# Optimization experiments

Hardware: AMD Instinct MI355X
Metric: run time of the kernel (lower is better)

The kernel has to match this reference:

```python
import jax, jax.numpy as jnp
import numpy as np

D_EMBED = 1024


def setup_inputs() -> dict:
    key = jax.random.key(0)
    ks = jax.random.split(key, 8)
    B, S, D = 8, 2048, D_EMBED
    scale = 1.0 / np.sqrt(D)
    return {
        "embeddings": jax.random.normal(ks[0], (B, S, D), dtype=jnp.float32),
        "mask": jnp.zeros((B, S, S), dtype=jnp.float32),
        "Wq": jax.random.normal(ks[1], (D, D), dtype=jnp.float32) * scale,
        "bq": jax.random.normal(ks[2], (D,), dtype=jnp.float32) * 0.02,
        "Wk": jax.random.normal(ks[3], (D, D), dtype=jnp.float32) * scale,
        "bk": jax.random.normal(ks[4], (D,), dtype=jnp.float32) * 0.02,
        "Wv": jax.random.normal(ks[5], (D, D), dtype=jnp.float32) * scale,
        "bv": jax.random.normal(ks[6], (D,), dtype=jnp.float32) * 0.02,
    }


def reference(embeddings, mask, Wq, bq, Wk, bk, Wv, bv):
    # torch Linear: y = x @ W.T + b
    q = jnp.einsum('bsd,ed->bse', embeddings, Wq) + bq
    k = jnp.einsum('bsd,ed->bse', embeddings, Wk) + bk
    v = jnp.einsum('bsd,ed->bse', embeddings, Wv) + bv
    scores = jnp.einsum('bqd,bkd->bqk', q, k)
    # NOTE: faithful to source — mask added BEFORE scaling by 1/sqrt(d)
    scores = (scores + mask) * (1.0 / jnp.sqrt(jnp.float32(q.shape[-1])))
    attn = jax.nn.softmax(scores, axis=-1)
    return jnp.einsum('bqk,bkd->bqd', attn, v)
```

## Files before the change

### kernel.cpp

```cpp
#include <hip/hip_runtime.h>


#define B_SZ 8
#define SEQ  2048
#define DIM  1024
#define MROWS (B_SZ * SEQ)

typedef unsigned short u16;
typedef short short8 __attribute__((ext_vector_type(8)));
typedef unsigned short u16x4 __attribute__((ext_vector_type(4)));
typedef float f32x4 __attribute__((ext_vector_type(4)));

__device__ __forceinline__ u16 f2h(float x) {
  _Float16 h = (_Float16)x;
  union { _Float16 f; u16 u; } c; c.f = h; return c.u;
}
__device__ __forceinline__ float h2f(u16 u) {
  union { _Float16 f; u16 u; } c; c.u = u; return (float)c.f;
}

__device__ __forceinline__ int xcd_swz(int x, int nwg) {
  return (x & 7) * (nwg >> 3) + (x >> 3);
}

__device__ __forceinline__ void gload_lds16(const u16* g, u16* l) {
  __builtin_amdgcn_global_load_lds(
      (__attribute__((address_space(1))) void*)(g),
      (__attribute__((address_space(3))) void*)(l), 16, 0, 0);
}

__device__ __forceinline__ f32x4 mfma_f16(short8 a, short8 b, f32x4 c) {
  asm("v_mfma_f32_16x16x32_f16 %0, %1, %2, %0" : "+v"(c) : "v"(a), "v"(b));
  return c;
}

__device__ __forceinline__ void gemm256_core(const u16* __restrict__ Ag,
                                             const u16* __restrict__ Bg,
                                             int NT, size_t lda, size_t ldb,
                                             u16* sm, f32x4 (&acc)[8][4]) {
  const int tid = threadIdx.x;
  const int lane = tid & 63;
  const int wid = tid >> 6;
  const int wm8 = (wid >> 2) << 3;
  const int wn4 = (wid & 3) << 2;

  u16* sA = sm;
  u16* sB = sm + 32768;

  const int bb = (lane << 4) ^ (((lane >> 5) & 1) << 5);
  const int rins = bb >> 6;
  const int cins = (bb & 63) >> 1;
  const int s0 = wid, s1 = 8 + wid, s2 = 16 + wid, s3 = 24 + wid;
  const size_t aoff0 = (size_t)((s0 >> 1) * 16 + rins) * lda + ((s0 & 1) * 32 + cins);
  const size_t aoff1 = (size_t)((s1 >> 1) * 16 + rins) * lda + ((s1 & 1) * 32 + cins);
  const size_t aoff2 = (size_t)((s2 >> 1) * 16 + rins) * lda + ((s2 & 1) * 32 + cins);
  const size_t aoff3 = (size_t)((s3 >> 1) * 16 + rins) * lda + ((s3 & 1) * 32 + cins);
  const size_t boff0 = (size_t)((s0 >> 1) * 16 + rins) * ldb + ((s0 & 1) * 32 + cins);
  const size_t boff1 = (size_t)((s1 >> 1) * 16 + rins) * ldb + ((s1 & 1) * 32 + cins);
  const size_t boff2 = (size_t)((s2 >> 1) * 16 + rins) * ldb + ((s2 & 1) * 32 + cins);
  const size_t boff3 = (size_t)((s3 >> 1) * 16 + rins) * ldb + ((s3 & 1) * 32 + cins);
  const int wid512 = wid << 9;

  const int lof = ((lane & 15) << 6) + ((lane >> 4) << 4);
  const int loe = (lof ^ (((lane >> 3) & 1) << 5)) >> 1;

#define ISSUE_A(j, nb, kt) \
  gload_lds16(Ag + aoff##j + (size_t)(kt) * 64, sA + (nb) * 16384 + (j) * 4096 + wid512)
#define ISSUE_B(j, nb, kt) \
  gload_lds16(Bg + boff##j + (size_t)(kt) * 64, sB + (nb) * 16384 + (j) * 4096 + wid512)

  ISSUE_B(0, 0, 0); ISSUE_B(1, 0, 0); ISSUE_B(2, 0, 0); ISSUE_B(3, 0, 0);
  ISSUE_A(0, 0, 0); ISSUE_A(2, 0, 0); ISSUE_A(1, 0, 0); ISSUE_A(3, 0, 0);

  int buf = 0;
  for (int kt = 0; kt < NT; ++kt) {
    const int nk = kt + 1;
    const bool pre = nk < NT;
    const int nb = buf ^ 1;
    asm volatile("s_waitcnt vmcnt(2)" ::: "memory");
    __builtin_amdgcn_s_barrier();
    asm volatile("" ::: "memory");
    const u16* bufA = sA + buf * 16384;
    const u16* bufB = sB + buf * 16384;
    short8 bf[4][2];
#pragma unroll
    for (int n = 0; n < 4; ++n) {
      bf[n][0] = *(const short8*)(bufB + (wn4 + n) * 1024 + loe);
      bf[n][1] = *(const short8*)(bufB + (wn4 + n) * 1024 + 512 + loe);
    }
    {
      short8 af[2][2];
#pragma unroll
      for (int m = 0; m < 2; ++m) {
        af[m][0] = *(const short8*)(bufA + (wm8 + m) * 1024 + loe);
        af[m][1] = *(const short8*)(bufA + (wm8 + m) * 1024 + 512 + loe);
      }
      if (pre) {
        ISSUE_B(0, nb, nk); ISSUE_B(1, nb, nk); ISSUE_B(2, nb, nk); ISSUE_B(3, nb, nk);
        ISSUE_A(0, nb, nk); ISSUE_A(2, nb, nk); ISSUE_A(1, nb, nk); ISSUE_A(3, nb, nk);
      }
      __builtin_amdgcn_s_setprio(1);
#pragma unroll
      for (int m = 0; m < 2; ++m)
#pragma unroll
        for (int n = 0; n < 4; ++n) {
          acc[m][n] = mfma_f16(af[m][0], bf[n][0], acc[m][n]);
          acc[m][n] = mfma_f16(af[m][1], bf[n][1], acc[m][n]);
        }
      __builtin_amdgcn_s_setprio(0);
    }
    {
      short8 af[2][2];
#pragma unroll
      for (int m = 0; m < 2; ++m) {
        af[m][0] = *(const short8*)(bufA + (wm8 + 2 + m) * 1024 + loe);
        af[m][1] = *(const short8*)(bufA + (wm8 + 2 + m) * 1024 + 512 + loe);
      }
      __builtin_amdgcn_s_setprio(1);
#pragma unroll
      for (int m = 0; m < 2; ++m)
#pragma unroll
        for (int n = 0; n < 4; ++n) {
          acc[2 + m][n] = mfma_f16(af[m][0], bf[n][0], acc[2 + m][n]);
          acc[2 + m][n] = mfma_f16(af[m][1], bf[n][1], acc[2 + m][n]);
        }
      __builtin_amdgcn_s_setprio(0);
    }
    if (pre) {
      asm volatile("s_waitcnt vmcnt(8)" ::: "memory");
    } else {
      asm volatile("s_waitcnt vmcnt(0)" ::: "memory");
    }
    __builtin_amdgcn_s_barrier();
    asm volatile("" ::: "memory");
    {
      short8 af[2][2];
#pragma unroll
      for (int m = 0; m < 2; ++m) {
        af[m][0] = *(const short8*)(bufA + (wm8 + 4 + m) * 1024 + loe);
        af[m][1] = *(const short8*)(bufA + (wm8 + 4 + m) * 1024 + 512 + loe);
      }
      __builtin_amdgcn_s_setprio(1);
#pragma unroll
      for (int m = 0; m < 2; ++m)
#pragma unroll
        for (int n = 0; n < 4; ++n) {
          acc[4 + m][n] = mfma_f16(af[m][0], bf[n][0], acc[4 + m][n]);
          acc[4 + m][n] = mfma_f16(af[m][1], bf[n][1], acc[4 + m][n]);
        }
      __builtin_amdgcn_s_setprio(0);
    }
    {
      short8 af[2][2];
#pragma unroll
      for (int m = 0; m < 2; ++m) {
        af[m][0] = *(const short8*)(bufA + (wm8 + 6 + m) * 1024 + loe);
        af[m][1] = *(const short8*)(bufA + (wm8 + 6 + m) * 1024 + 512 + loe);
      }
      __builtin_amdgcn_s_setprio(1);
#pragma unroll
      for (int m = 0; m < 2; ++m)
#pragma unroll
        for (int n = 0; n < 4; ++n) {
          acc[6 + m][n] = mfma_f16(af[m][0], bf[n][0], acc[6 + m][n]);
          acc[6 + m][n] = mfma_f16(af[m][1], bf[n][1], acc[6 + m][n]);
        }
      __builtin_amdgcn_s_setprio(0);
    }
    buf ^= 1;
  }
  asm volatile("s_nop 7\n\ts_nop 7\n\ts_nop 7" ::);
#undef ISSUE_A
#undef ISSUE_B
}

__device__ __forceinline__ void gemm128_core(const u16* A, const u16* Bt, int K,
                                             int lda, int ldb, f32x4 (&acc)[4][4],
                                             u16* sA, u16* sB) {
  const int tid = threadIdx.x;
  const int lane = tid & 63;
  const int wid = tid >> 6;
  const int wr = wid >> 1;
  const int wc = wid & 1;
  const int srow = tid >> 2;
  const int scol = (tid & 3) << 3;
  const u16* ga0 = A + (size_t)srow * lda + scol;
  const u16* ga1 = A + (size_t)(srow + 64) * lda + scol;
  const u16* gb0 = Bt + (size_t)srow * ldb + scol;
  const u16* gb1 = Bt + (size_t)(srow + 64) * ldb + scol;
  u16* la0 = sA + (wid << 9);
  u16* la1 = sA + 2048 + (wid << 9);
  u16* lb0 = sB + (wid << 9);
  u16* lb1 = sB + 2048 + (wid << 9);
  const u16* pa = sA + (size_t)((wr << 6) + (lane & 15)) * 32 + ((lane >> 4) << 3);
  const u16* pb = sB + (size_t)((wc << 6) + (lane & 15)) * 32 + ((lane >> 4) << 3);
  const int ksteps = K >> 5;
  for (int kt = 0; kt < ksteps; ++kt) {
    gload_lds16(ga0, la0);
    gload_lds16(ga1, la1);
    gload_lds16(gb0, lb0);
    gload_lds16(gb1, lb1);
    ga0 += 32; ga1 += 32; gb0 += 32; gb1 += 32;
    __syncthreads();
    short8 a[4], b[4];
#pragma unroll
    for (int i = 0; i < 4; ++i) a[i] = *(const short8*)(pa + (i << 9));
#pragma unroll
    for (int i = 0; i < 4; ++i) b[i] = *(const short8*)(pb + (i << 9));
#pragma unroll
    for (int mi = 0; mi < 4; ++mi)
#pragma unroll
      for (int ni = 0; ni < 4; ++ni)
        acc[mi][ni] = mfma_f16(a[mi], b[ni], acc[mi][ni]);
    __syncthreads();
  }
  asm volatile("s_nop 7\n\ts_nop 7\n\ts_nop 7" ::);
}

__global__ __launch_bounds__(256) void cvt_kernel(const float* __restrict__ in,
                                                  u16* __restrict__ out, int n4) {
  int i = blockIdx.x * 256 + threadIdx.x;
  if (i >= n4) return;
  float4 v = ((const float4*)in)[i];
  u16x4 o;
  o[0] = f2h(v.x); o[1] = f2h(v.y); o[2] = f2h(v.z); o[3] = f2h(v.w);
  ((u16x4*)out)[i] = o;
}

__global__ __launch_bounds__(256) void cvt_wT_kernel(const float* __restrict__ Wq,
                                                     const float* __restrict__ Wk,
                                                     u16* __restrict__ WqT,
                                                     u16* __restrict__ WkT) {
  __shared__ float t[64][65];
  const float* src = blockIdx.z ? Wk : Wq;
  u16* dst = blockIdx.z ? WkT : WqT;
  const int r0 = blockIdx.x * 64;
  const int c0 = blockIdx.y * 64;
  const int tid = threadIdx.x;
  const int tr = tid >> 4;
  const int c4 = (tid & 15) << 2;
#pragma unroll
  for (int i = 0; i < 4; ++i) {
    float4 x = *(const float4*)(src + (size_t)(r0 + tr + 16 * i) * 1024 + c0 + c4);
    t[tr + 16 * i][c4 + 0] = x.x;
    t[tr + 16 * i][c4 + 1] = x.y;
    t[tr + 16 * i][c4 + 2] = x.z;
    t[tr + 16 * i][c4 + 3] = x.w;
  }
  __syncthreads();
#pragma unroll
  for (int i = 0; i < 4; ++i) {
    int dr = tr + 16 * i;
    u16x4 y;
    y[0] = f2h(t[c4 + 0][dr]);
    y[1] = f2h(t[c4 + 1][dr]);
    y[2] = f2h(t[c4 + 2][dr]);
    y[3] = f2h(t[c4 + 3][dr]);
    *(u16x4*)(dst + (size_t)(c0 + dr) * 1024 + r0 + c4) = y;
  }
}

__global__ __launch_bounds__(256) void mtw_kernel(const u16* __restrict__ WqT,
                                                  const u16* __restrict__ WkT,
                                                  const float* __restrict__ bq,
                                                  u16* __restrict__ Mt,
                                                  float* __restrict__ w) {
  __shared__ __align__(16) u16 sA[128 * 32];
  __shared__ __align__(16) u16 sB[128 * 32];
  const int b = blockIdx.x;
  if (b < 64) {
    const int m0 = (b >> 3) * 128;
    const int n0 = (b & 7) * 128;
    f32x4 acc[4][4] = {};
    gemm128_core(WkT + (size_t)m0 * 1024, WqT + (size_t)n0 * 1024, 1024, 1024, 1024,
                 acc, sA, sB);
    const int lane = threadIdx.x & 63, wid = threadIdx.x >> 6;
    const int wr = wid >> 1, wc = wid & 1;
#pragma unroll
    for (int mi = 0; mi < 4; ++mi)
#pragma unroll
      for (int ni = 0; ni < 4; ++ni)
#pragma unroll
        for (int j = 0; j < 4; ++j) {
          int row = m0 + (wr << 6) + mi * 16 + ((lane >> 4) << 2) + j;
          int col = n0 + (wc << 6) + ni * 16 + (lane & 15);
          Mt[(size_t)row * 1024 + col] = f2h(acc[mi][ni][j] * 0.03125f);
        }
  } else {
    const int e = (b - 64) * 256 + threadIdx.x;
    const u16* row = WkT + (size_t)e * 1024;
    float s = 0.f;
    for (int d = 0; d < 1024; d += 8) {
      short8 v = *(const short8*)(row + d);
#pragma unroll
      for (int j = 0; j < 8; ++j) s += h2f((u16)v[j]) * bq[d + j];
    }
    w[e] = s * 0.03125f;
  }
}

__global__ __launch_bounds__(256) void c_kernel(const u16* __restrict__ emb16,
                                                const float* __restrict__ w,
                                                float* __restrict__ c) {
  __shared__ float sw[1024];
  for (int i = threadIdx.x; i < 1024; i += 256) sw[i] = w[i];
  __syncthreads();
  const int r = blockIdx.x * 256 + threadIdx.x;
  const u16* row = emb16 + (size_t)r * 1024;
  float s = 0.f;
  for (int d = 0; d < 1024; d += 8) {
    short8 v = *(const short8*)(row + d);
#pragma unroll
    for (int j = 0; j < 8; ++j) s += h2f((u16)v[j]) * sw[d + j];
  }
  c[r] = s;
}

__global__ __launch_bounds__(512) void proj256_kernel(const u16* __restrict__ emb16,
                                                      const u16* __restrict__ Mt,
                                                      const u16* __restrict__ Wv16,
                                                      const float* __restrict__ bv,
                                                      u16* __restrict__ G,
                                                      u16* __restrict__ vT) {
  __shared__ __align__(16) u16 sm[65536];
  const int wg = xcd_swz(blockIdx.x, 512);
  const int lane = threadIdx.x & 63, wid = threadIdx.x >> 6;
  f32x4 acc[8][4] = {};
  if (wg < 256) {
    const int m0 = (wg >> 2) * 256;
    const int n0 = (wg & 3) * 256;
    gemm256_core(emb16 + (size_t)m0 * 1024, Mt + (size_t)n0 * 1024, 16, 1024, 1024,
                 sm, acc);
    const int rb = m0 + ((wid >> 2) << 7) + ((lane >> 4) << 2);
    const int cb = n0 + ((wid & 3) << 6) + (lane & 15);
#pragma unroll
    for (int m = 0; m < 8; ++m)
#pragma unroll
      for (int n = 0; n < 4; ++n)
#pragma unroll
        for (int j = 0; j < 4; ++j)
          G[(size_t)(rb + m * 16 + j) * 1024 + (cb + n * 16)] = f2h(acc[m][n][j]);
  } else {
    const int r = wg - 256;
    const int m0 = (r & 3) * 256;
    const int n0 = (r >> 2) * 256;
    gemm256_core(Wv16 + (size_t)m0 * 1024, emb16 + (size_t)n0 * 1024, 16, 1024, 1024,
                 sm, acc);
    const int rb = m0 + ((wid >> 2) << 7) + ((lane >> 4) << 2);
    const int cb = n0 + ((wid & 3) << 6) + (lane & 15);
#pragma unroll
    for (int m = 0; m < 8; ++m)
#pragma unroll
      for (int n = 0; n < 4; ++n)
#pragma unroll
        for (int j = 0; j < 4; ++j) {
          int d = rb + m * 16 + j;
          int kg = cb + n * 16;
          int bi = kg >> 11, s = kg & 2047;
          vT[((size_t)bi << 21) + ((size_t)d << 11) + s] = f2h(acc[m][n][j] + bv[d]);
        }
  }
}

__global__ __launch_bounds__(512) void scores256_kernel(const u16* __restrict__ G,
                                                        const u16* __restrict__ emb16,
                                                        const float* __restrict__ c,
                                                        u16* __restrict__ scH) {
  __shared__ __align__(16) u16 sm[65536];
  const int wg = xcd_swz(blockIdx.x, 512);
  const int b = wg >> 6;
  const int m0 = ((wg >> 3) & 7) * 256;
  const int n0 = (wg & 7) * 256;
  f32x4 acc[8][4] = {};
  gemm256_core(G + ((size_t)b * SEQ + m0) * DIM, emb16 + ((size_t)b * SEQ + n0) * DIM,
               16, DIM, DIM, sm, acc);
  const int lane = threadIdx.x & 63, wid = threadIdx.x >> 6;
  const int rb = m0 + ((wid >> 2) << 7) + ((lane >> 4) << 2);
  const int cb = n0 + ((wid & 3) << 6) + (lane & 15);
  float cn[4];
#pragma unroll
  for (int n = 0; n < 4; ++n) cn[n] = c[(size_t)b * SEQ + cb + n * 16];
#pragma unroll
  for (int m = 0; m < 8; ++m)
#pragma unroll
    for (int n = 0; n < 4; ++n)
#pragma unroll
      for (int j = 0; j < 4; ++j) {
        size_t idx = ((size_t)b * SEQ + rb + m * 16 + j) * SEQ + (cb + n * 16);
        scH[idx] = f2h(acc[m][n][j] + cn[n]);
      }
}

__global__ __launch_bounds__(256) void softmax_kernel(u16* __restrict__ scH,
                                                      const float* __restrict__ mask) {
  __shared__ float red[8];
  const size_t row = blockIdx.x;
  u16* rowp = scH + row * SEQ;
  const float* mrow = mask + row * SEQ;
  const int tid = threadIdx.x;
  short8 raw = *(const short8*)(rowp + tid * 8);
  float4 m0 = ((const float4*)mrow)[2 * tid];
  float4 m1 = ((const float4*)mrow)[2 * tid + 1];
  float mk[8] = {m0.x, m0.y, m0.z, m0.w, m1.x, m1.y, m1.z, m1.w};
  float f[8];
#pragma unroll
  for (int j = 0; j < 8; ++j) f[j] = h2f((u16)raw[j]) + mk[j] * 0.03125f;
  float mx = f[0];
#pragma unroll
  for (int j = 1; j < 8; ++j) mx = fmaxf(mx, f[j]);
#pragma unroll
  for (int off = 1; off < 64; off <<= 1) mx = fmaxf(mx, __shfl_xor(mx, off));
  const int wid = tid >> 6, lane = tid & 63;
  if (lane == 0) red[wid] = mx;
  __syncthreads();
  mx = fmaxf(fmaxf(red[0], red[1]), fmaxf(red[2], red[3]));
  float e[8];
  float s = 0.f;
#pragma unroll
  for (int j = 0; j < 8; ++j) {
    e[j] = __expf(f[j] - mx);
    s += e[j];
  }
#pragma unroll
  for (int off = 1; off < 64; off <<= 1) s += __shfl_xor(s, off);
  if (lane == 0) red[4 + wid] = s;
  __syncthreads();
  s = (red[4] + red[5]) + (red[6] + red[7]);
  const float inv = 1.f / s;
  short8 o;
#pragma unroll
  for (int j = 0; j < 8; ++j) o[j] = (short)f2h(e[j] * inv);
  *(short8*)(rowp + tid * 8) = o;
}

__global__ __launch_bounds__(512) void pv256_kernel(const u16* __restrict__ pr,
                                                    const u16* __restrict__ vt,
                                                    float* __restrict__ out) {
  __shared__ __align__(16) u16 sm[65536];
  const int wg = xcd_swz(blockIdx.x, 256);
  const int b = wg >> 5;
  const int m0 = ((wg >> 2) & 7) * 256;
  const int n0 = (wg & 3) * 256;
  f32x4 acc[8][4] = {};
  gemm256_core(pr + ((size_t)b * SEQ + m0) * SEQ, vt + ((size_t)b * DIM + n0) * SEQ,
               32, SEQ, SEQ, sm, acc);
  const int lane = threadIdx.x & 63, wid = threadIdx.x >> 6;
  const int rb = m0 + ((wid >> 2) << 7) + ((lane >> 4) << 2);
  const int cb = n0 + ((wid & 3) << 6) + (lane & 15);
#pragma unroll
  for (int m = 0; m < 8; ++m)
#pragma unroll
    for (int n = 0; n < 4; ++n)
#pragma unroll
      for (int j = 0; j < 4; ++j)
        out[((size_t)b * SEQ + rb + m * 16 + j) * DIM + (cb + n * 16)] = acc[m][n][j];
}

extern "C" void kernel_launch(void* const* d_in, const int* in_sizes, int n_in,
                              void* d_out, int out_size, void* d_ws, size_t ws_size,
                              hipStream_t stream) {
  const float* emb  = (const float*)d_in[0];
  const float* mask = (const float*)d_in[1];
  const float* Wq   = (const float*)d_in[2];
  const float* bq   = (const float*)d_in[3];
  const float* Wk   = (const float*)d_in[4];
  const float* bk   = (const float*)d_in[5];
  const float* Wv   = (const float*)d_in[6];
  const float* bv   = (const float*)d_in[7];
  float* out = (float*)d_out;
  (void)bk;

  const size_t M1 = 1024 * 1024;
  u16* scH   = (u16*)d_ws;
  u16* emb16 = scH + 32 * M1;
  u16* WqT   = emb16 + 16 * M1;
  u16* WkT   = WqT + M1;
  u16* Wv16  = WkT + M1;
  u16* Mt    = Wv16 + M1;
  u16* G     = Mt + M1;
  u16* vT    = G + 16 * M1;
  float* w   = (float*)(vT + 16 * M1);
  float* c   = w + 1024;

  cvt_kernel<<<16384, 256, 0, stream>>>(emb, emb16, (int)(4 * M1));
  cvt_wT_kernel<<<dim3(16, 16, 2), 256, 0, stream>>>(Wq, Wk, WqT, WkT);
  cvt_kernel<<<1024, 256, 0, stream>>>(Wv, Wv16, (int)(M1 / 4));

  mtw_kernel<<<68, 256, 0, stream>>>(WqT, WkT, bq, Mt, w);
  c_kernel<<<64, 256, 0, stream>>>(emb16, w, c);

  proj256_kernel<<<512, 512, 0, stream>>>(emb16, Mt, Wv16, bv, G, vT);

  scores256_kernel<<<512, 512, 0, stream>>>(G, emb16, c, scH);
  softmax_kernel<<<MROWS, 256, 0, stream>>>(scH, mask);
  pv256_kernel<<<256, 512, 0, stream>>>((const u16*)scH, vT, out);
}
```

Measured before the change: 335.0 us.

## Fuse prep kernels, split-K the Mt GEMM, and parallelize c reduction per wavefront

Merges the three conversion kernels and the w = Wk^T·bq dot product into one prep launch, computing w directly from fp32 Wk with coalesced column reads. The small 64-block Mt GEMM is split four ways over K and run in the same launch as the c reduction. The c reduction now uses one wavefront per row with shuffle reduction instead of one thread per row. A new reduction kernel sums the fp32 partial planes into Mt. The aim is to cut launch count and raise occupancy in the under-parallelized setup stages, at the cost of extra fp32 partial traffic and an extra launch.

```diff
diff --git a/kernel.cpp b/kernel.cpp
--- a/kernel.cpp
+++ b/kernel.cpp
@@ -217,65 +217,112 @@
   asm volatile("s_nop 7\n\ts_nop 7\n\ts_nop 7" ::);
 }
 
-__global__ __launch_bounds__(256) void cvt_kernel(const float* __restrict__ in,
-                                                  u16* __restrict__ out, int n4) {
-  int i = blockIdx.x * 256 + threadIdx.x;
-  if (i >= n4) return;
-  float4 v = ((const float4*)in)[i];
-  u16x4 o;
-  o[0] = f2h(v.x); o[1] = f2h(v.y); o[2] = f2h(v.z); o[3] = f2h(v.w);
-  ((u16x4*)out)[i] = o;
-}
-
-__global__ __launch_bounds__(256) void cvt_wT_kernel(const float* __restrict__ Wq,
-                                                     const float* __restrict__ Wk,
-                                                     u16* __restrict__ WqT,
-                                                     u16* __restrict__ WkT) {
+__global__ __launch_bounds__(256) void prep_kernel(const float* __restrict__ emb,
+                                                   const float* __restrict__ Wq,
+                                                   const float* __restrict__ Wk,
+                                                   const float* __restrict__ Wv,
+                                                   const float* __restrict__ bq,
+                                                   u16* __restrict__ emb16,
+                                                   u16* __restrict__ WqT,
+                                                   u16* __restrict__ WkT,
+                                                   u16* __restrict__ Wv16,
+                                                   float* __restrict__ w) {
   __shared__ float t[64][65];
-  const float* src = blockIdx.z ? Wk : Wq;
-  u16* dst = blockIdx.z ? WkT : WqT;
-  const int r0 = blockIdx.x * 64;
-  const int c0 = blockIdx.y * 64;
+  const int b = blockIdx.x;
   const int tid = threadIdx.x;
-  const int tr = tid >> 4;
-  const int c4 = (tid & 15) << 2;
-#pragma unroll
-  for (int i = 0; i < 4; ++i) {
-    float4 x = *(const float4*)(src + (size_t)(r0 + tr + 16 * i) * 1024 + c0 + c4);
-    t[tr + 16 * i][c4 + 0] = x.x;
-    t[tr + 16 * i][c4 + 1] = x.y;
-    t[tr + 16 * i][c4 + 2] = x.z;
-    t[tr + 16 * i][c4 + 3] = x.w;
+  if (b < 16384) {
+    int i = b * 256 + tid;
+    float4 v = ((const float4*)emb)[i];
+    u16x4 o;
+    o[0] = f2h(v.x); o[1] = f2h(v.y); o[2] = f2h(v.z); o[3] = f2h(v.w);
+    ((u16x4*)emb16)[i] = o;
+  } else if (b < 16896) {
+    const int b2 = b - 16384;
+    const float* src = (b2 >> 8) ? Wk : Wq;
+    u16* dst = (b2 >> 8) ? WkT : WqT;
+    const int rem = b2 & 255;
+    const int r0 = (rem >> 4) * 64;
+    const int c0 = (rem & 15) * 64;
+    const int tr = tid >> 4;
+    const int c4 = (tid & 15) << 2;
+#pragma unroll
+    for (int i = 0; i < 4; ++i) {
+      float4 x = *(const float4*)(src + (size_t)(r0 + tr + 16 * i) * 1024 + c0 + c4);
+      t[tr + 16 * i][c4 + 0] = x.x;
+      t[tr + 16 * i][c4 + 1] = x.y;
+      t[tr + 16 * i][c4 + 2] = x.z;
+      t[tr + 16 * i][c4 + 3] = x.w;
+    }
+    __syncthreads();
+#pragma unroll
+    for (int i = 0; i < 4; ++i) {
+      int dr = tr + 16 * i;
+      u16x4 y;
+      y[0] = f2h(t[c4 + 0][dr]);
+      y[1] = f2h(t[c4 + 1][dr]);
+      y[2] = f2h(t[c4 + 2][dr]);
+      y[3] = f2h(t[c4 + 3][dr]);
+      *(u16x4*)(dst + (size_t)(c0 + dr) * 1024 + r0 + c4) = y;
+    }
+  } else if (b < 17920) {
+    int i = (b - 16896) * 256 + tid;
+    float4 v = ((const float4*)Wv)[i];
+    u16x4 o;
+    o[0] = f2h(v.x); o[1] = f2h(v.y); o[2] = f2h(v.z); o[3] = f2h(v.w);
+    ((u16x4*)Wv16)[i] = o;
+  } else {
+    const int e = (b - 17920) * 256 + tid;
+    float s = 0.f;
+    for (int c = 0; c < 1024; c += 4) {
+      s += Wk[(size_t)c * 1024 + e] * bq[c];
+      s += Wk[(size_t)(c + 1) * 1024 + e] * bq[c + 1];
+      s += Wk[(size_t)(c + 2) * 1024 + e] * bq[c + 2];
+      s += Wk[(size_t)(c + 3) * 1024 + e] * bq[c + 3];
+    }
+    w[e] = s * 0.03125f;
   }
-  __syncthreads();
-#pragma unroll
-  for (int i = 0; i < 4; ++i) {
-    int dr = tr + 16 * i;
-    u16x4 y;
-    y[0] = f2h(t[c4 + 0][dr]);
-    y[1] = f2h(t[c4 + 1][dr]);
-    y[2] = f2h(t[c4 + 2][dr]);
-    y[3] = f2h(t[c4 + 3][dr]);
-    *(u16x4*)(dst + (size_t)(c0 + dr) * 1024 + r0 + c4) = y;
-  }
-}
-
-__global__ __launch_bounds__(256) void mtw_kernel(const u16* __restrict__ WqT,
+}
+
+__global__ __launch_bounds__(256) void cmt_kernel(const u16* __restrict__ emb16,
+                                                  const u16* __restrict__ WqT,
                                                   const u16* __restrict__ WkT,
-                                                  const float* __restrict__ bq,
-                                                  u16* __restrict__ Mt,
-                                                  float* __restrict__ w) {
-  __shared__ __align__(16) u16 sA[128 * 32];
-  __shared__ __align__(16) u16 sB[128 * 32];
+                                                  const float* __restrict__ w,
+                                                  float* __restrict__ c,
+                                                  float* __restrict__ MtP) {
+  __shared__ __align__(16) u16 smem[8192];
   const int b = blockIdx.x;
-  if (b < 64) {
-    const int m0 = (b >> 3) * 128;
-    const int n0 = (b & 7) * 128;
+  const int tid = threadIdx.x;
+  if (b < 4096) {
+    float* sw = (float*)smem;
+    for (int i = tid; i < 1024; i += 256) sw[i] = w[i];
+    __syncthreads();
+    const int wv = tid >> 6, lane = tid & 63;
+    const int r = b * 4 + wv;
+    const u16* row = emb16 + (size_t)r * 1024;
+    float s = 0.f;
+#pragma unroll
+    for (int it = 0; it < 2; ++it) {
+      int d = lane * 8 + it * 512;
+      short8 v = *(const short8*)(row + d);
+#pragma unroll
+      for (int j = 0; j < 8; ++j) s += h2f((u16)v[j]) * sw[d + j];
+    }
+#pragma unroll
+    for (int off = 1; off < 64; off <<= 1) s += __shfl_xor(s, off);
+    if (lane == 0) c[r] = s;
+  } else {
+    const int b2 = b - 4096;
+    const int tile = b2 >> 2;
+    const int kc = b2 & 3;
+    const int m0 = (tile >> 3) * 128;
+    const int n0 = (tile & 7) * 128;
     f32x4 acc[4][4] = {};
-    gemm128_core(WkT + (size_t)m0 * 1024, WqT + (size_t)n0 * 1024, 1024, 1024, 1024,
-                 acc, sA, sB);
-    const int lane = threadIdx.x & 63, wid = threadIdx.x >> 6;
+    gemm128_core(WkT + (size_t)m0 * 1024 + kc * 256,
+                 WqT + (size_t)n0 * 1024 + kc * 256, 256, 1024, 1024,
+                 acc, smem, smem + 4096);
+    const int lane = tid & 63, wid = tid >> 6;
     const int wr = wid >> 1, wc = wid & 1;
+    float* plane = MtP + (size_t)kc * 1024 * 1024;
 #pragma unroll
     for (int mi = 0; mi < 4; ++mi)
 #pragma unroll
@@ -284,36 +331,24 @@
         for (int j = 0; j < 4; ++j) {
           int row = m0 + (wr << 6) + mi * 16 + ((lane >> 4) << 2) + j;
           int col = n0 + (wc << 6) + ni * 16 + (lane & 15);
-          Mt[(size_t)row * 1024 + col] = f2h(acc[mi][ni][j] * 0.03125f);
+          plane[(size_t)row * 1024 + col] = acc[mi][ni][j];
         }
-  } else {
-    const int e = (b - 64) * 256 + threadIdx.x;
-    const u16* row = WkT + (size_t)e * 1024;
-    float s = 0.f;
-    for (int d = 0; d < 1024; d += 8) {
-      short8 v = *(const short8*)(row + d);
-#pragma unroll
-      for (int j = 0; j < 8; ++j) s += h2f((u16)v[j]) * bq[d + j];
-    }
-    w[e] = s * 0.03125f;
   }
 }
 
-__global__ __launch_bounds__(256) void c_kernel(const u16* __restrict__ emb16,
-                                                const float* __restrict__ w,
-                                                float* __restrict__ c) {
-  __shared__ float sw[1024];
-  for (int i = threadIdx.x; i < 1024; i += 256) sw[i] = w[i];
-  __syncthreads();
-  const int r = blockIdx.x * 256 + threadIdx.x;
-  const u16* row = emb16 + (size_t)r * 1024;
-  float s = 0.f;
-  for (int d = 0; d < 1024; d += 8) {
-    short8 v = *(const short8*)(row + d);
-#pragma unroll
-    for (int j = 0; j < 8; ++j) s += h2f((u16)v[j]) * sw[d + j];
-  }
-  c[r] = s;
+__global__ __launch_bounds__(256) void mtred_kernel(const float* __restrict__ MtP,
+                                                    u16* __restrict__ Mt) {
+  const size_t i = (size_t)blockIdx.x * 1024 + threadIdx.x * 4;
+  float4 a = *(const float4*)(MtP + i);
+  float4 b = *(const float4*)(MtP + 1048576 + i);
+  float4 cc = *(const float4*)(MtP + 2097152 + i);
+  float4 d = *(const float4*)(MtP + 3145728 + i);
+  u16x4 o;
+  o[0] = f2h((a.x + b.x + cc.x + d.x) * 0.03125f);
+  o[1] = f2h((a.y + b.y + cc.y + d.y) * 0.03125f);
+  o[2] = f2h((a.z + b.z + cc.z + d.z) * 0.03125f);
+  o[3] = f2h((a.w + b.w + cc.w + d.w) * 0.03125f);
+  *(u16x4*)(Mt + i) = o;
 }
 
 __global__ __launch_bounds__(512) void proj256_kernel(const u16* __restrict__ emb16,
@@ -479,15 +514,13 @@
   u16* Mt    = Wv16 + M1;
   u16* G     = Mt + M1;
   u16* vT    = G + 16 * M1;
-  float* w   = (float*)(vT + 16 * M1);
+  float* MtP = (float*)(vT + 16 * M1);
+  float* w   = MtP + 4 * M1;
   float* c   = w + 1024;
 
-  cvt_kernel<<<16384, 256, 0, stream>>>(emb, emb16, (int)(4 * M1));
-  cvt_wT_kernel<<<dim3(16, 16, 2), 256, 0, stream>>>(Wq, Wk, WqT, WkT);
-  cvt_kernel<<<1024, 256, 0, stream>>>(Wv, Wv16, (int)(M1 / 4));
-
-  mtw_kernel<<<68, 256, 0, stream>>>(WqT, WkT, bq, Mt, w);
-  c_kernel<<<64, 256, 0, stream>>>(emb16, w, c);
+  prep_kernel<<<17924, 256, 0, stream>>>(emb, Wq, Wk, Wv, bq, emb16, WqT, WkT, Wv16, w);
+  cmt_kernel<<<4352, 256, 0, stream>>>(emb16, WqT, WkT, w, c, MtP);
+  mtred_kernel<<<1024, 256, 0, stream>>>(MtP, Mt);
 
   proj256_kernel<<<512, 512, 0, stream>>>(emb16, Mt, Wv16, bv, G, vT);
 
```

Result: no change. 328.8 us (-1.9%).
